# Kernel optimization log

Hardware: AMD Instinct MI355X
Metric: run time of the kernel (lower is better)

## Reference

```python
import jax, jax.numpy as jnp
import numpy as np

TEMPERATURE = 0.1


def setup_inputs() -> dict:
    key = jax.random.key(0)
    k1, k2 = jax.random.split(key)
    N, D = 8192, 128
    features = jax.random.normal(k1, (N, D), dtype=jnp.float32)
    labels = jax.random.randint(k2, (N,), 0, 1000, dtype=jnp.int64)
    return {"features": features, "labels": labels}


def reference(features, labels):
    N = features.shape[0]
    # L2-normalize rows
    feats = features / jnp.linalg.norm(features, axis=1, keepdims=True)
    # positive-pair mask from labels [N, N]
    labels = labels.reshape(-1, 1)
    mask = (labels == labels.T).astype(feats.dtype)
    # similarity matrix scaled by temperature
    sim = jnp.matmul(feats, feats.T) / TEMPERATURE
    # exclude self-comparisons (diagonal)
    logits_mask = 1.0 - jnp.eye(N, dtype=feats.dtype)
    mask = mask * logits_mask
    exp_logits = jnp.exp(sim) * logits_mask
    log_prob = sim - jnp.log(exp_logits.sum(axis=1, keepdims=True) + 1e-9)
    mask_sum = mask.sum(axis=1)
    mask_sum = jnp.where(mask_sum == 0, jnp.ones_like(mask_sum), mask_sum)
    mean_log_prob_pos = (mask * log_prob).sum(axis=1) / mask_sum
    return -mean_log_prob_pos.mean()
```

## Files before the change

kernel.cpp:

```cpp
#include <hip/hip_runtime.h>
#include <hip/hip_bf16.h>
#include <math.h>


constexpr int N = 8192;
constexpr int D = 128;

typedef __attribute__((ext_vector_type(8))) short short8;
typedef __attribute__((ext_vector_type(4))) float f32x4;

__device__ __forceinline__ float fast_exp2(float x) {
#if __has_builtin(__builtin_amdgcn_exp2f)
    return __builtin_amdgcn_exp2f(x);
#else
    return __expf(x * 0.69314718056f);
#endif
}

__device__ __forceinline__ void gload_lds16(const void* g, void* s) {
    __builtin_amdgcn_global_load_lds(
        (const __attribute__((address_space(1))) unsigned int*)g,
        (__attribute__((address_space(3))) unsigned int*)s, 16, 0, 0);
}

__global__ void prep_kernel(const float* __restrict__ F,
                            unsigned short* __restrict__ Fb,
                            float* __restrict__ out) {
    int row = blockIdx.x * 16 + (threadIdx.x >> 6);
    int l = threadIdx.x & 63;
    float2 v = ((const float2*)(F + (size_t)row * D))[l];
    float ss = v.x * v.x + v.y * v.y;
#pragma unroll
    for (int off = 32; off > 0; off >>= 1) ss += __shfl_xor(ss, off);
    float sc = sqrtf(14.4269504089f / ss);
    __hip_bfloat16 hx = __float2bfloat16(v.x * sc);
    __hip_bfloat16 hy = __float2bfloat16(v.y * sc);
    ushort2 u;
    u.x = *(unsigned short*)&hx;
    u.y = *(unsigned short*)&hy;
    ((ushort2*)(Fb + (size_t)row * D))[l] = u;
    if (blockIdx.x == 0 && threadIdx.x == 0) out[0] = 0.0f;
}

__device__ __forceinline__ void stage_tile64(const unsigned short* __restrict__ src,
                                             unsigned short* dst,
                                             int w, int lr, int lq) {
#pragma unroll
    for (int it = 0; it < 4; ++it) {
        int a = it * 4 + w;
        int r = a * 4 + lr;
        int q = lq ^ (r & 7);
        gload_lds16(src + (size_t)r * D + q * 8, dst + a * 512);
    }
}

__global__ __launch_bounds__(256, 4) void sim_kernel(
    const unsigned short* __restrict__ Fb, const int* __restrict__ labels,
    float* __restrict__ pE, float* __restrict__ pP) {
    __shared__ unsigned short Bt[2][64 * D];

    const int chunk = blockIdx.x;
    const int bb = blockIdx.y;
    const int i0 = bb * 128;
    const int t = threadIdx.x, w = t >> 6, l = t & 63;
    const int c = l & 15, quad = l >> 4;

    short8 af[2][4];
    int li[2][4];
#pragma unroll
    for (int mb = 0; mb < 2; ++mb) {
        const unsigned short* ar = Fb + (size_t)(i0 + w * 32 + mb * 16 + c) * D;
#pragma unroll
        for (int kk = 0; kk < 4; ++kk)
            af[mb][kk] = *(const short8*)(ar + (kk * 4 + quad) * 8);
#pragma unroll
        for (int r = 0; r < 4; ++r)
            li[mb][r] = labels[i0 + w * 32 + mb * 16 + quad * 4 + r];
    }

    stage_tile64(Fb + (size_t)(chunk * 8) * 64 * D, Bt[0], w, quad, c);

    float RE[2][4] = {}, RP[2][4] = {};
    const int myjt = bb * 2 + (w >> 1);

    for (int s = 0; s < 8; ++s) {
        const int jt = chunk * 8 + s, j0 = jt * 64, p = s & 1;
        __syncthreads();
        if (s < 7)
            stage_tile64(Fb + (size_t)(jt + 1) * 64 * D, Bt[p ^ 1], w, quad, c);

        int lj[4];
#pragma unroll
        for (int n = 0; n < 4; ++n) lj[n] = labels[j0 + n * 16 + c];

        f32x4 acc[2][4] = {};
#pragma unroll
        for (int kk = 0; kk < 4; ++kk) {
            int sl = (kk * 4 + quad) ^ (c & 7);
            short8 bf[4];
#pragma unroll
            for (int n = 0; n < 4; ++n)
                bf[n] = *(const short8*)&Bt[p][(n * 16 + c) * D + sl * 8];
#pragma unroll
            for (int mb = 0; mb < 2; ++mb)
#pragma unroll
                for (int n = 0; n < 4; ++n)
                    acc[mb][n] = __builtin_amdgcn_mfma_f32_16x16x32_bf16(
                        af[mb][kk], bf[n], acc[mb][n], 0, 0, 0);
        }

        if (jt == myjt) {
#pragma unroll
            for (int mb = 0; mb < 2; ++mb)
#pragma unroll
                for (int n = 0; n < 4; ++n)
#pragma unroll
                    for (int r = 0; r < 4; ++r) {
                        float s2 = acc[mb][n][r];
                        bool self = ((w & 1) * 32 + mb * 16 + quad * 4 + r) ==
                                    (n * 16 + c);
                        bool pos = (li[mb][r] == lj[n]) && !self;
                        RE[mb][r] += self ? 0.0f : fast_exp2(s2);
                        RP[mb][r] += pos ? s2 : 0.0f;
                    }
        } else {
#pragma unroll
            for (int mb = 0; mb < 2; ++mb)
#pragma unroll
                for (int n = 0; n < 4; ++n)
#pragma unroll
                    for (int r = 0; r < 4; ++r) {
                        float s2 = acc[mb][n][r];
                        RE[mb][r] += fast_exp2(s2);
                        RP[mb][r] += (li[mb][r] == lj[n]) ? s2 : 0.0f;
                    }
        }
    }

#pragma unroll
    for (int mb = 0; mb < 2; ++mb)
#pragma unroll
        for (int r = 0; r < 4; ++r) {
#pragma unroll
            for (int off = 1; off < 16; off <<= 1) {
                RE[mb][r] += __shfl_xor(RE[mb][r], off);
                RP[mb][r] += __shfl_xor(RP[mb][r], off);
            }
        }
    if (c == 0) {
#pragma unroll
        for (int mb = 0; mb < 2; ++mb)
#pragma unroll
            for (int r = 0; r < 4; ++r) {
                int row = i0 + w * 32 + mb * 16 + quad * 4 + r;
                pE[row * 16 + chunk] = RE[mb][r];
                pP[row * 16 + chunk] = RP[mb][r];
            }
    }
}

__global__ void finalize_kernel(const float* __restrict__ pE,
                                const float* __restrict__ pP,
                                const int* __restrict__ labels,
                                float* __restrict__ out) {
    __shared__ int h[1024];
    int t = threadIdx.x;
#pragma unroll
    for (int i = 0; i < 4; ++i) h[t + i * 256] = 0;
    __syncthreads();
    for (int i = t; i < N; i += 256) atomicAdd(&h[labels[i]], 1);
    __syncthreads();

    float a = 0.0f;
    if (t < 64) {
        int row = blockIdx.x * 64 + t;
        int cnt = h[labels[row]] - 1;
        if (cnt > 0) {
            const float4* e = (const float4*)(pE + (size_t)row * 16);
            const float4* p = (const float4*)(pP + (size_t)row * 16);
            float E = 0.0f, P = 0.0f;
#pragma unroll
            for (int i = 0; i < 4; ++i) {
                float4 ev = e[i], pv = p[i];
                E += (ev.x + ev.y) + (ev.z + ev.w);
                P += (pv.x + pv.y) + (pv.z + pv.w);
            }
            a = __logf(E + 1e-9f) - 0.69314718056f * P / (float)cnt;
        }
#pragma unroll
        for (int off = 32; off > 0; off >>= 1) a += __shfl_xor(a, off);
        if (t == 0) atomicAdd(out, a * (1.0f / (float)N));
    }
}

extern "C" void kernel_launch(void* const* d_in, const int* in_sizes, int n_in,
                              void* d_out, int out_size, void* d_ws, size_t ws_size,
                              hipStream_t stream) {
    const float* F      = (const float*)d_in[0];
    const int*   labels = (const int*)d_in[1];
    float* out = (float*)d_out;

    unsigned short* Fb = (unsigned short*)d_ws;
    float* pE = (float*)(Fb + (size_t)N * D);
    float* pP = pE + (size_t)N * 16;

    prep_kernel<<<N / 16, 1024, 0, stream>>>(F, Fb, out);
    sim_kernel<<<dim3(16, 64), 256, 0, stream>>>(Fb, labels, pE, pP);
    finalize_kernel<<<128, 256, 0, stream>>>(pE, pP, labels, out);
}
```

Before: 106.9 us.

## Use 256x256 tiles with whole B chunk staged once, single-block finalize

The similarity kernel now uses 512-thread blocks covering a 256-row by 256-column tile. The entire 256-row B chunk (64 KB of LDS) is loaded once up front instead of double-buffering 64-row tiles, and the inner loop runs 4 steps with no per-step barriers. Partial sums are stored column-major per chunk, and the finalize kernel becomes a single 1024-thread block that reduces all 32 partials and writes the output directly, removing the atomic and the zero-init in prep. In exchange, load/compute overlap inside the sim kernel is lost, the larger LDS footprint may cut occupancy, and the final reduction is serialized into one block.

```diff
diff --git a/kernel.cpp b/kernel.cpp
--- a/kernel.cpp
+++ b/kernel.cpp
@@ -24,8 +24,7 @@
 }
 
 __global__ void prep_kernel(const float* __restrict__ F,
-                            unsigned short* __restrict__ Fb,
-                            float* __restrict__ out) {
+                            unsigned short* __restrict__ Fb) {
     int row = blockIdx.x * 16 + (threadIdx.x >> 6);
     int l = threadIdx.x & 63;
     float2 v = ((const float2*)(F + (size_t)row * D))[l];
@@ -39,32 +38,33 @@
     u.x = *(unsigned short*)&hx;
     u.y = *(unsigned short*)&hy;
     ((ushort2*)(Fb + (size_t)row * D))[l] = u;
-    if (blockIdx.x == 0 && threadIdx.x == 0) out[0] = 0.0f;
-}
-
-__device__ __forceinline__ void stage_tile64(const unsigned short* __restrict__ src,
-                                             unsigned short* dst,
-                                             int w, int lr, int lq) {
-#pragma unroll
-    for (int it = 0; it < 4; ++it) {
-        int a = it * 4 + w;
+}
+
+__device__ __forceinline__ void stage_chunk(const unsigned short* __restrict__ src,
+                                            unsigned short* dst, int w, int l) {
+    int lr = l >> 4, lq = l & 15;
+#pragma unroll
+    for (int it = 0; it < 8; ++it) {
+        int a = w * 8 + it;
         int r = a * 4 + lr;
         int q = lq ^ (r & 7);
         gload_lds16(src + (size_t)r * D + q * 8, dst + a * 512);
     }
 }
 
-__global__ __launch_bounds__(256, 4) void sim_kernel(
+__global__ __launch_bounds__(512, 4) void sim_kernel(
     const unsigned short* __restrict__ Fb, const int* __restrict__ labels,
     float* __restrict__ pE, float* __restrict__ pP) {
-    __shared__ unsigned short Bt[2][64 * D];
+    __shared__ unsigned short Bt[256 * D];
 
     const int chunk = blockIdx.x;
-    const int bb = blockIdx.y;
-    const int i0 = bb * 128;
+    const int rb = blockIdx.y;
+    const int i0 = rb * 256, j0 = chunk * 256;
     const int t = threadIdx.x, w = t >> 6, l = t & 63;
     const int c = l & 15, quad = l >> 4;
 
+    stage_chunk(Fb + (size_t)j0 * D, Bt, w, l);
+
     short8 af[2][4];
     int li[2][4];
 #pragma unroll
@@ -78,20 +78,17 @@
             li[mb][r] = labels[i0 + w * 32 + mb * 16 + quad * 4 + r];
     }
 
-    stage_tile64(Fb + (size_t)(chunk * 8) * 64 * D, Bt[0], w, quad, c);
+    __syncthreads();
 
     float RE[2][4] = {}, RP[2][4] = {};
-    const int myjt = bb * 2 + (w >> 1);
-
-    for (int s = 0; s < 8; ++s) {
-        const int jt = chunk * 8 + s, j0 = jt * 64, p = s & 1;
-        __syncthreads();
-        if (s < 7)
-            stage_tile64(Fb + (size_t)(jt + 1) * 64 * D, Bt[p ^ 1], w, quad, c);
-
+    const bool diagBlk = (chunk == rb);
+
+#pragma unroll 1
+    for (int s = 0; s < 4; ++s) {
+        const int jb = s * 64;
         int lj[4];
 #pragma unroll
-        for (int n = 0; n < 4; ++n) lj[n] = labels[j0 + n * 16 + c];
+        for (int n = 0; n < 4; ++n) lj[n] = labels[j0 + jb + n * 16 + c];
 
         f32x4 acc[2][4] = {};
 #pragma unroll
@@ -100,7 +97,7 @@
             short8 bf[4];
 #pragma unroll
             for (int n = 0; n < 4; ++n)
-                bf[n] = *(const short8*)&Bt[p][(n * 16 + c) * D + sl * 8];
+                bf[n] = *(const short8*)&Bt[(jb + n * 16 + c) * D + sl * 8];
 #pragma unroll
             for (int mb = 0; mb < 2; ++mb)
 #pragma unroll
@@ -109,7 +106,7 @@
                         af[mb][kk], bf[n], acc[mb][n], 0, 0, 0);
         }
 
-        if (jt == myjt) {
+        if (diagBlk && s == (w >> 1)) {
 #pragma unroll
             for (int mb = 0; mb < 2; ++mb)
 #pragma unroll
@@ -153,8 +150,8 @@
 #pragma unroll
             for (int r = 0; r < 4; ++r) {
                 int row = i0 + w * 32 + mb * 16 + quad * 4 + r;
-                pE[row * 16 + chunk] = RE[mb][r];
-                pP[row * 16 + chunk] = RP[mb][r];
+                pE[(size_t)chunk * N + row] = RE[mb][r];
+                pP[(size_t)chunk * N + row] = RP[mb][r];
             }
     }
 }
@@ -164,32 +161,36 @@
                                 const int* __restrict__ labels,
                                 float* __restrict__ out) {
     __shared__ int h[1024];
+    __shared__ float ws16[16];
     int t = threadIdx.x;
-#pragma unroll
-    for (int i = 0; i < 4; ++i) h[t + i * 256] = 0;
-    __syncthreads();
-    for (int i = t; i < N; i += 256) atomicAdd(&h[labels[i]], 1);
+    h[t] = 0;
+    __syncthreads();
+    for (int i = t; i < N; i += 1024) atomicAdd(&h[labels[i]], 1);
     __syncthreads();
 
     float a = 0.0f;
-    if (t < 64) {
-        int row = blockIdx.x * 64 + t;
+#pragma unroll 1
+    for (int k = 0; k < 8; ++k) {
+        int row = t + k * 1024;
         int cnt = h[labels[row]] - 1;
-        if (cnt > 0) {
-            const float4* e = (const float4*)(pE + (size_t)row * 16);
-            const float4* p = (const float4*)(pP + (size_t)row * 16);
-            float E = 0.0f, P = 0.0f;
-#pragma unroll
-            for (int i = 0; i < 4; ++i) {
-                float4 ev = e[i], pv = p[i];
-                E += (ev.x + ev.y) + (ev.z + ev.w);
-                P += (pv.x + pv.y) + (pv.z + pv.w);
-            }
-            a = __logf(E + 1e-9f) - 0.69314718056f * P / (float)cnt;
-        }
-#pragma unroll
-        for (int off = 32; off > 0; off >>= 1) a += __shfl_xor(a, off);
-        if (t == 0) atomicAdd(out, a * (1.0f / (float)N));
+        float E = 0.0f, P = 0.0f;
+#pragma unroll
+        for (int ch = 0; ch < 32; ++ch) {
+            E += pE[(size_t)ch * N + row];
+            P += pP[(size_t)ch * N + row];
+        }
+        if (cnt > 0)
+            a += __logf(E + 1e-9f) - 0.69314718056f * P / (float)cnt;
+    }
+#pragma unroll
+    for (int off = 32; off > 0; off >>= 1) a += __shfl_xor(a, off);
+    if ((t & 63) == 0) ws16[t >> 6] = a;
+    __syncthreads();
+    if (t == 0) {
+        float s = 0.0f;
+#pragma unroll
+        for (int i = 0; i < 16; ++i) s += ws16[i];
+        out[0] = s / (float)N;
     }
 }
 
@@ -202,9 +203,9 @@
 
     unsigned short* Fb = (unsigned short*)d_ws;
     float* pE = (float*)(Fb + (size_t)N * D);
-    float* pP = pE + (size_t)N * 16;
-
-    prep_kernel<<<N / 16, 1024, 0, stream>>>(F, Fb, out);
-    sim_kernel<<<dim3(16, 64), 256, 0, stream>>>(Fb, labels, pE, pP);
-    finalize_kernel<<<128, 256, 0, stream>>>(pE, pP, labels, out);
-}
+    float* pP = pE + (size_t)32 * N;
+
+    prep_kernel<<<N / 16, 1024, 0, stream>>>(F, Fb);
+    sim_kernel<<<dim3(32, 32), 512, 0, stream>>>(Fb, labels, pE, pP);
+    finalize_kernel<<<1, 1024, 0, stream>>>(pE, pP, labels, out);
+}
```

New measurement: 111.9 us. +4.8%, slower.
